# Performance work log

Hardware: AMD Instinct MI355X
Metric: run time of the kernel (lower is better)

## Reference

```python
import jax, jax.numpy as jnp
import numpy as np

B, S, H = 2, 2048, 2048
NUM_HEADS, HEAD_DIM, GROUP_SIZE = 16, 128, 4
NUM_KV_HEADS = NUM_HEADS // GROUP_SIZE
ROPE_THETA = 10000.0


def setup_inputs() -> dict:
    key = jax.random.key(0)
    ks = jax.random.split(key, 10)
    xavier = lambda k, fi, fo: jax.random.uniform(k, (fi, fo), jnp.float32,
                                                  -jnp.sqrt(6.0 / (fi + fo)), jnp.sqrt(6.0 / (fi + fo)))
    hidden_states = jax.random.normal(ks[0], (B, S, H), jnp.float32)
    # causal mask: 1.0 where attention is disallowed (strictly upper triangle)
    mask = jnp.triu(jnp.ones((S, S), jnp.float32), k=1)[None, None, :, :]
    mask = jnp.broadcast_to(mask, (B, 1, S, S))
    return {
        "hidden_states": hidden_states,
        "mask": mask,
        "Wq": xavier(ks[1], H, NUM_HEADS * HEAD_DIM), "bq": jnp.zeros((NUM_HEADS * HEAD_DIM,), jnp.float32),
        "Wk": xavier(ks[2], H, NUM_KV_HEADS * HEAD_DIM), "bk": jnp.zeros((NUM_KV_HEADS * HEAD_DIM,), jnp.float32),
        "Wv": xavier(ks[3], H, NUM_KV_HEADS * HEAD_DIM), "bv": jnp.zeros((NUM_KV_HEADS * HEAD_DIM,), jnp.float32),
        "Wo": xavier(ks[4], NUM_HEADS * HEAD_DIM, H), "bo": jnp.zeros((H,), jnp.float32),
    }


def _apply_rope(q, k):
    # q: [b, s, hq, d], k: [b, s, hk, d]
    s, d = q.shape[1], q.shape[-1]
    inv_freq = 1.0 / (ROPE_THETA ** (jnp.arange(0, d, 2, dtype=jnp.float32) / d))  # [d/2]
    angles = jnp.arange(s, dtype=jnp.float32)[:, None] * inv_freq[None, :]          # [s, d/2]
    cos = jnp.cos(angles)[None, :, None, :]  # [1, s, 1, d/2]
    sin = jnp.sin(angles)[None, :, None, :]

    def rot(x):
        x1, x2 = jnp.split(x, 2, axis=-1)
        return jnp.concatenate([x1 * cos - x2 * sin, x1 * sin + x2 * cos], axis=-1)

    return rot(q), rot(k)


def reference(hidden_states, mask, Wq, bq, Wk, bk, Wv, bv, Wo, bo):
    b, s, _ = hidden_states.shape
    scale = 1.0 / jnp.sqrt(jnp.float32(HEAD_DIM))

    q = (hidden_states @ Wq + bq).reshape(b, s, NUM_HEADS, HEAD_DIM)
    k = (hidden_states @ Wk + bk).reshape(b, s, NUM_KV_HEADS, HEAD_DIM)
    v = (hidden_states @ Wv + bv).reshape(b, s, NUM_KV_HEADS, HEAD_DIM)

    q, k = _apply_rope(q, k)

    q = jnp.transpose(q, (0, 2, 1, 3))  # [b, hq, s, d]
    k = jnp.transpose(k, (0, 2, 1, 3))  # [b, hk, s, d]
    v = jnp.transpose(v, (0, 2, 1, 3))

    new_past_key, new_past_value = k, v

    # GQA: repeat each KV head group_size times
    k_rep = jnp.repeat(k, GROUP_SIZE, axis=1)  # [b, hq, s, d]
    v_rep = jnp.repeat(v, GROUP_SIZE, axis=1)

    attn_scores = jnp.einsum('bhqd,bhkd->bhqk', q, k_rep) * scale  # [b, hq, s, s]
    attn_scores = attn_scores + mask * -1e9
    attn_probs = jax.nn.softmax(attn_scores, axis=-1)
    attn_output = jnp.einsum('bhqk,bhkd->bhqd', attn_probs, v_rep)

    attn_output = attn_output.transpose(0, 2, 1, 3).reshape(b, s, NUM_HEADS * HEAD_DIM)
    attn_output = attn_output @ Wo + bo
    return attn_output, new_past_key, new_past_value
```

## Files before the change

### kernel.cpp

```cpp
#include <hip/hip_runtime.h>
#include <stdint.h>

#define S_LEN 2048
#define HDIM  2048
#define N_HEADS 16
#define HEAD_D 128
#define N_KV 4

typedef unsigned short u16;
typedef __attribute__((ext_vector_type(8))) short bf16x8;
typedef __attribute__((ext_vector_type(4))) short bf16x4;
typedef __attribute__((ext_vector_type(4))) float f32x4;

#define MFMA_PV(a, b, c) __builtin_amdgcn_mfma_f32_16x16x16bf16_1k(a, b, c, 0, 0, 0)

__device__ __forceinline__ u16 f2bf(float f) {
  unsigned u = __float_as_uint(f);
  u += 0x7FFFu + ((u >> 16) & 1u);
  return (u16)(u >> 16);
}

__device__ __forceinline__ void gll16(void* lds, const void* gp) {
  __builtin_amdgcn_global_load_lds(
      (const __attribute__((address_space(1))) void*)gp,
      (__attribute__((address_space(3))) void*)lds, 16, 0, 0);
}

__global__ __launch_bounds__(256) void k_convert(const float* __restrict__ src,
                                                 u16* __restrict__ dst, int n4) {
  int i = blockIdx.x * 256 + threadIdx.x;
  if (i < n4) {
    float4 v = ((const float4*)src)[i];
    ushort4 o;
    o.x = f2bf(v.x); o.y = f2bf(v.y); o.z = f2bf(v.z); o.w = f2bf(v.w);
    ((ushort4*)dst)[i] = o;
  }
}

__global__ __launch_bounds__(256) void k_transpose_w(const float* __restrict__ W,
                                                     u16* __restrict__ Wt,
                                                     int K, int N) {
  __shared__ float tile[64][65];
  int k0 = blockIdx.x * 64, n0 = blockIdx.y * 64;
  int tr = threadIdx.x >> 6, tc = threadIdx.x & 63;
#pragma unroll
  for (int i = 0; i < 16; ++i) {
    int r = tr + i * 4;
    tile[r][tc] = W[(size_t)(k0 + r) * N + n0 + tc];
  }
  __syncthreads();
#pragma unroll
  for (int i = 0; i < 16; ++i) {
    int r = tr + i * 4;
    Wt[(size_t)(n0 + r) * K + k0 + tc] = f2bf(tile[tc][r]);
  }
}

__device__ __forceinline__ void gemm_tile_128(
    const u16* __restrict__ A, const u16* __restrict__ Bt,
    const float* __restrict__ bias, float* __restrict__ C,
    int m0, int n0, int K, int ldc) {
  __shared__ __align__(16) u16 sA[128 * 32];
  __shared__ __align__(16) u16 sB[128 * 32];
  const int tid = threadIdx.x;
  const int lane = tid & 63;
  const int wave = tid >> 6;
  const int quad = lane >> 4;
  const int l15 = lane & 15;
  const int wm = (wave >> 1) << 6;
  const int wn = (wave & 1) << 6;

  f32x4 acc[4][4];
#pragma unroll
  for (int i = 0; i < 4; ++i)
#pragma unroll
    for (int j = 0; j < 4; ++j)
      acc[i][j] = (f32x4){0.f, 0.f, 0.f, 0.f};

  for (int kk = 0; kk < K; kk += 32) {
    __syncthreads();
#pragma unroll
    for (int it = 0; it < 2; ++it) {
      int c = tid + (it << 8);
      int row = c >> 2;
      int ko = (c & 3) << 3;
      gll16((char*)sA + c * 16, A + (size_t)(m0 + row) * K + kk + ko);
      gll16((char*)sB + c * 16, Bt + (size_t)(n0 + row) * K + kk + ko);
    }
    __syncthreads();
    bf16x8 af[4], bfr[4];
#pragma unroll
    for (int i = 0; i < 4; ++i)
      af[i] = *(const bf16x8*)&sA[(wm + (i << 4) + l15) * 32 + quad * 8];
#pragma unroll
    for (int j = 0; j < 4; ++j)
      bfr[j] = *(const bf16x8*)&sB[(wn + (j << 4) + l15) * 32 + quad * 8];
#pragma unroll
    for (int i = 0; i < 4; ++i)
#pragma unroll
      for (int j = 0; j < 4; ++j)
        acc[i][j] = __builtin_amdgcn_mfma_f32_16x16x32_bf16(af[i], bfr[j], acc[i][j], 0, 0, 0);
  }

#pragma unroll
  for (int i = 0; i < 4; ++i) {
    int row = m0 + wm + (i << 4) + quad * 4;
#pragma unroll
    for (int j = 0; j < 4; ++j) {
      int col = n0 + wn + (j << 4) + l15;
      float bv = bias[col];
      float* cp = C + (size_t)row * ldc + col;
#pragma unroll
      for (int r = 0; r < 4; ++r)
        cp[(size_t)r * ldc] = acc[i][j][r] + bv;
    }
  }
}

__global__ __launch_bounds__(256) void k_gemm_qkv(
    const u16* __restrict__ X, const u16* __restrict__ Wqt,
    const u16* __restrict__ Wkt, const u16* __restrict__ Wvt,
    const float* __restrict__ bq, const float* __restrict__ bk,
    const float* __restrict__ bv, float* __restrict__ Qf,
    float* __restrict__ Kf, float* __restrict__ Vf) {
  int m0 = blockIdx.x << 7;
  int by = blockIdx.y;
  const u16* Bt; const float* bias; float* C; int n0, ldc;
  if (by < 16)      { Bt = Wqt; bias = bq; C = Qf; n0 = by << 7;        ldc = 2048; }
  else if (by < 20) { Bt = Wkt; bias = bk; C = Kf; n0 = (by - 16) << 7; ldc = 512;  }
  else              { Bt = Wvt; bias = bv; C = Vf; n0 = (by - 20) << 7; ldc = 512;  }
  gemm_tile_128(X, Bt, bias, C, m0, n0, 2048, ldc);
}

__global__ __launch_bounds__(256) void k_gemm_o(
    const u16* __restrict__ A, const u16* __restrict__ Wot,
    const float* __restrict__ bo, float* __restrict__ C) {
  gemm_tile_128(A, Wot, bo, C, blockIdx.x << 7, blockIdx.y << 7, 2048, 2048);
}

__global__ __launch_bounds__(256) void k_rope(
    const float* __restrict__ Qf, const float* __restrict__ Kf,
    u16* __restrict__ Qbf, u16* __restrict__ Kbf, float* __restrict__ outK) {
  const int bx = blockIdx.x;
  const int b = bx >> 11;
  const int s = bx & 2047;
  const int tid = threadIdx.x;
  const float qscale = 0.08838834764831845f * 1.4426950408889634f;
  const float c1 = -13.287712379549449f / 64.f;

#pragma unroll
  for (int it = 0; it < 4; ++it) {
    int p = tid + (it << 8);
    int hh = p >> 6;
    int ii = p & 63;
    float ang = (float)s * exp2f((float)ii * c1);
    float cs, sn;
    sincosf(ang, &sn, &cs);
    const float* src = Qf + (size_t)bx * 2048 + hh * 128 + ii;
    float x1 = src[0], x2 = src[64];
    float o1 = (x1 * cs - x2 * sn) * qscale;
    float o2 = (x1 * sn + x2 * cs) * qscale;
    u16* dst = Qbf + ((size_t)(b * N_HEADS + hh) * S_LEN + s) * HEAD_D + ii;
    dst[0] = f2bf(o1);
    dst[64] = f2bf(o2);
  }
  {
    int hh = tid >> 6;
    int ii = tid & 63;
    float ang = (float)s * exp2f((float)ii * c1);
    float cs, sn;
    sincosf(ang, &sn, &cs);
    const float* src = Kf + (size_t)bx * 512 + hh * 128 + ii;
    float x1 = src[0], x2 = src[64];
    float o1 = x1 * cs - x2 * sn;
    float o2 = x1 * sn + x2 * cs;
    size_t idx = ((size_t)(b * N_KV + hh) * S_LEN + s) * HEAD_D + ii;
    Kbf[idx] = f2bf(o1);
    Kbf[idx + 64] = f2bf(o2);
    outK[idx] = o1;
    outK[idx + 64] = o2;
  }
}

__global__ __launch_bounds__(256) void k_vtrans(const float* __restrict__ Vf,
                                                u16* __restrict__ Vt,
                                                float* __restrict__ outV) {
  __shared__ float tile[64][65];
  int s0 = blockIdx.x * 64, d0 = blockIdx.y * 64;
  int z = blockIdx.z;
  int b = z >> 2, kvh = z & 3;
  int tr = threadIdx.x >> 6, tc = threadIdx.x & 63;
#pragma unroll
  for (int i = 0; i < 16; ++i) {
    int r = tr + i * 4;
    float v = Vf[(size_t)(b * S_LEN + s0 + r) * 512 + kvh * 128 + d0 + tc];
    tile[r][tc] = v;
    outV[((size_t)z * S_LEN + s0 + r) * HEAD_D + d0 + tc] = v;
  }
  __syncthreads();
#pragma unroll
  for (int i = 0; i < 16; ++i) {
    int r = tr + i * 4;
    Vt[((size_t)z * HEAD_D + d0 + r) * S_LEN + s0 + tc] = f2bf(tile[tc][r]);
  }
}

__global__ __launch_bounds__(256, 2) void k_attn(
    const u16* __restrict__ Qbf, const u16* __restrict__ Kbf,
    const u16* __restrict__ Vt, u16* __restrict__ attn) {
  __shared__ __align__(16) u16 smem[17920];
  u16* sK = smem;
  u16* sV = smem + 8704;

  const int tid = threadIdx.x;
  const int lane = tid & 63;
  const int wave = tid >> 6;
  const int quad = lane >> 4;
  const int l15 = lane & 15;

  const int by = blockIdx.y;
  const int qt = (by < 8) ? (15 - 2 * by) : (2 * (by - 8));
  const int bh = blockIdx.x;
  const int b = bh >> 4;
  const int h = bh & 15;
  const int kvh = h >> 2;
  const int q0 = qt << 7;
  const int qw = q0 + wave * 32;

  const u16* Qb = Qbf + ((size_t)(b * N_HEADS + h) * S_LEN + qw) * HEAD_D;
  const u16* Kb = Kbf + (size_t)(b * N_KV + kvh) * S_LEN * HEAD_D;
  const u16* Vb = Vt + (size_t)(b * N_KV + kvh) * HEAD_D * S_LEN;

  bf16x8 aq[2][4];
#pragma unroll
  for (int i = 0; i < 2; ++i)
#pragma unroll
    for (int kc = 0; kc < 4; ++kc)
      aq[i][kc] = *(const bf16x8*)(Qb + (size_t)(i * 16 + l15) * HEAD_D + kc * 32 + quad * 8);

  float mst[2] = {-1e30f, -1e30f}, lst[2] = {0.f, 0.f};
  f32x4 oacc[2][8];
#pragma unroll
  for (int i = 0; i < 2; ++i)
#pragma unroll
    for (int n = 0; n < 8; ++n) oacc[i][n] = (f32x4){0.f, 0.f, 0.f, 0.f};

  const int ntiles = 2 * qt + 2;
  for (int t = 0; t < ntiles; ++t) {
    const int kt0 = t << 6;
    __syncthreads();
#pragma unroll
    for (int it = 0; it < 9; ++it) {
      int c = tid + (it << 8);
      if (c < 1088) {
        int row = c / 17;
        int k16 = c - row * 17;
        gll16((char*)sK + c * 16, Kb + (size_t)(kt0 + row) * HEAD_D + k16 * 8);
      } else if (c < 2240) {
        int vv = c - 1088;
        int d = vv / 9;
        int s16 = vv - d * 9;
        gll16((char*)sV + vv * 16, Vb + (size_t)d * S_LEN + kt0 + s16 * 8);
      }
    }
    __syncthreads();

    if (kt0 > qw + 31) continue;

    f32x4 st[2][4];
#pragma unroll
    for (int i = 0; i < 2; ++i)
#pragma unroll
      for (int j = 0; j < 4; ++j) st[i][j] = (f32x4){0.f, 0.f, 0.f, 0.f};
#pragma unroll
    for (int kc = 0; kc < 4; ++kc) {
#pragma unroll
      for (int j = 0; j < 4; ++j) {
        bf16x8 kf = *(const bf16x8*)&sK[(j * 16 + l15) * 136 + kc * 32 + quad * 8];
#pragma unroll
        for (int i = 0; i < 2; ++i)
          st[i][j] = __builtin_amdgcn_mfma_f32_16x16x32_bf16(kf, aq[i][kc], st[i][j], 0, 0, 0);
      }
    }

    if (kt0 + 63 > qw) {
#pragma unroll
      for (int i = 0; i < 2; ++i) {
        int q = qw + i * 16 + l15;
#pragma unroll
        for (int j = 0; j < 4; ++j) {
          int s = kt0 + j * 16 + quad * 4;
#pragma unroll
          for (int r = 0; r < 4; ++r)
            if (s + r > q) st[i][j][r] = -1e9f;
        }
      }
    }

    bf16x4 pf[2][4];
    float al[2];
#pragma unroll
    for (int i = 0; i < 2; ++i) {
      float m = -1e30f;
#pragma unroll
      for (int j = 0; j < 4; ++j)
#pragma unroll
        for (int r = 0; r < 4; ++r) m = fmaxf(m, st[i][j][r]);
      m = fmaxf(m, __shfl_xor(m, 16, 64));
      m = fmaxf(m, __shfl_xor(m, 32, 64));
      float mn = fmaxf(mst[i], m);
      al[i] = exp2f(mst[i] - mn);
      mst[i] = mn;
      float rs = 0.f;
#pragma unroll
      for (int j = 0; j < 4; ++j) {
#pragma unroll
        for (int r = 0; r < 4; ++r) {
          float p = exp2f(st[i][j][r] - mn);
          rs += p;
          pf[i][j][r] = (short)f2bf(p);
        }
      }
      rs += __shfl_xor(rs, 16, 64);
      rs += __shfl_xor(rs, 32, 64);
      lst[i] = lst[i] * al[i] + rs;
#pragma unroll
      for (int r = 0; r < 4; ++r) {
        float a = __shfl(al[i], quad * 4 + r, 16);
#pragma unroll
        for (int n = 0; n < 8; ++n) oacc[i][n][r] *= a;
      }
    }

#pragma unroll
    for (int j = 0; j < 4; ++j) {
#pragma unroll
      for (int n = 0; n < 8; ++n) {
        bf16x4 vf = *(const bf16x4*)&sV[(n * 16 + l15) * 72 + j * 16 + quad * 4];
#pragma unroll
        for (int i = 0; i < 2; ++i)
          oacc[i][n] = MFMA_PV(pf[i][j], vf, oacc[i][n]);
      }
    }
  }

#pragma unroll
  for (int i = 0; i < 2; ++i)
#pragma unroll
    for (int r = 0; r < 4; ++r) {
      float inv = 1.0f / __shfl(lst[i], quad * 4 + r, 16);
      int row = qw + i * 16 + quad * 4 + r;
      u16* op = attn + ((size_t)b * S_LEN + row) * HDIM + h * HEAD_D;
#pragma unroll
      for (int n = 0; n < 8; ++n)
        op[n * 16 + l15] = f2bf(oacc[i][n][r] * inv);
    }
}

extern "C" void kernel_launch(void* const* d_in, const int* in_sizes, int n_in,
                              void* d_out, int out_size, void* d_ws, size_t ws_size,
                              hipStream_t stream) {
  (void)in_sizes; (void)n_in; (void)out_size; (void)ws_size;
  const float* hs = (const float*)d_in[0];
  const float* Wq = (const float*)d_in[2];
  const float* bq = (const float*)d_in[3];
  const float* Wk = (const float*)d_in[4];
  const float* bk = (const float*)d_in[5];
  const float* Wv = (const float*)d_in[6];
  const float* bv = (const float*)d_in[7];
  const float* Wo = (const float*)d_in[8];
  const float* bo = (const float*)d_in[9];
  float* out = (float*)d_out;

  char* ws = (char*)d_ws;
  u16* Xbf   = (u16*)(ws + 0);
  u16* Wqt   = (u16*)(ws + 16777216);
  u16* Wkt   = (u16*)(ws + 25165824);
  u16* Wvt   = (u16*)(ws + 27262976);
  u16* Wot   = (u16*)(ws + 29360128);
  float* Qf  = (float*)(ws + 37748736);
  float* Kf  = (float*)(ws + 71303168);
  float* Vf  = (float*)(ws + 79691776);
  u16* Qbf   = (u16*)(ws + 88080384);
  u16* Kbf   = (u16*)(ws + 104857600);
  u16* Vtb   = (u16*)(ws + 109051904);
  u16* attnb = (u16*)(ws + 37748736);

  k_convert<<<8192, 256, 0, stream>>>(hs, Xbf, 2097152);
  k_transpose_w<<<dim3(32, 32), 256, 0, stream>>>(Wq, Wqt, 2048, 2048);
  k_transpose_w<<<dim3(32, 8), 256, 0, stream>>>(Wk, Wkt, 2048, 512);
  k_transpose_w<<<dim3(32, 8), 256, 0, stream>>>(Wv, Wvt, 2048, 512);
  k_transpose_w<<<dim3(32, 32), 256, 0, stream>>>(Wo, Wot, 2048, 2048);
  k_gemm_qkv<<<dim3(32, 24), 256, 0, stream>>>(Xbf, Wqt, Wkt, Wvt, bq, bk, bv, Qf, Kf, Vf);
  k_rope<<<4096, 256, 0, stream>>>(Qf, Kf, Qbf, Kbf, out + 8388608);
  k_vtrans<<<dim3(32, 2, 8), 256, 0, stream>>>(Vf, Vtb, out + 10485760);
  k_attn<<<dim3(32, 16), 256, 0, stream>>>(Qbf, Kbf, Vtb, attnb);
  k_gemm_o<<<dim3(32, 16), 256, 0, stream>>>(attnb, Wot, bo, out);
}
```

Measured before the change: 374.8 us.

## Split long causal attention tiles across two blocks and merge partials

Query tiles 8-15, which have the longest causal KV ranges, are split into two KV halves processed by separate blocks. Each half writes unnormalized bf16 partial outputs plus running max and sum, and a new combine kernel merges them. This balances the work per block and gives more blocks to fill the GPU. The cost is an extra kernel launch, partial-output traffic, and bf16 rounding of the partials. Separately, the softmax probabilities are now packed to bf16 with perm and round-half-up instead of round-to-nearest-even.

```diff
diff --git a/kernel.cpp b/kernel.cpp
--- a/kernel.cpp
+++ b/kernel.cpp
@@ -18,6 +18,10 @@
   unsigned u = __float_as_uint(f);
   u += 0x7FFFu + ((u >> 16) & 1u);
   return (u16)(u >> 16);
+}
+
+__device__ __forceinline__ float bf2f(u16 v) {
+  return __uint_as_float(((unsigned)v) << 16);
 }
 
 __device__ __forceinline__ void gll16(void* lds, const void* gp) {
@@ -207,7 +211,8 @@
 
 __global__ __launch_bounds__(256, 2) void k_attn(
     const u16* __restrict__ Qbf, const u16* __restrict__ Kbf,
-    const u16* __restrict__ Vt, u16* __restrict__ attn) {
+    const u16* __restrict__ Vt, u16* __restrict__ attn,
+    u16* __restrict__ pO, float* __restrict__ pML) {
   __shared__ __align__(16) u16 smem[17920];
   u16* sK = smem;
   u16* sV = smem + 8704;
@@ -219,7 +224,21 @@
   const int l15 = lane & 15;
 
   const int by = blockIdx.y;
-  const int qt = (by < 8) ? (15 - 2 * by) : (2 * (by - 8));
+  int qt, t0, t1, slot;
+  bool finalw;
+  if (by < 8) {
+    qt = 8 + by; t0 = 0; t1 = 16; finalw = false;
+    slot = ((blockIdx.x << 3) + (qt - 8)) << 1;
+  } else {
+    qt = 23 - by;
+    if (qt >= 8) {
+      t0 = 16; t1 = 2 * qt + 2; finalw = false;
+      slot = (((blockIdx.x << 3) + (qt - 8)) << 1) + 1;
+    } else {
+      t0 = 0; t1 = 2 * qt + 2; finalw = true; slot = 0;
+    }
+  }
+
   const int bh = blockIdx.x;
   const int b = bh >> 4;
   const int h = bh & 15;
@@ -245,8 +264,7 @@
 #pragma unroll
     for (int n = 0; n < 8; ++n) oacc[i][n] = (f32x4){0.f, 0.f, 0.f, 0.f};
 
-  const int ntiles = 2 * qt + 2;
-  for (int t = 0; t < ntiles; ++t) {
+  for (int t = t0; t < t1; ++t) {
     const int kt0 = t << 6;
     __syncthreads();
 #pragma unroll
@@ -314,12 +332,17 @@
       float rs = 0.f;
 #pragma unroll
       for (int j = 0; j < 4; ++j) {
-#pragma unroll
-        for (int r = 0; r < 4; ++r) {
-          float p = exp2f(st[i][j][r] - mn);
-          rs += p;
-          pf[i][j][r] = (short)f2bf(p);
-        }
+        float p0 = exp2f(st[i][j][0] - mn);
+        float p1 = exp2f(st[i][j][1] - mn);
+        float p2 = exp2f(st[i][j][2] - mn);
+        float p3 = exp2f(st[i][j][3] - mn);
+        rs += (p0 + p1) + (p2 + p3);
+        union { unsigned u[2]; bf16x4 v; } pk;
+        pk.u[0] = __builtin_amdgcn_perm(__float_as_uint(p1) + 0x8000u,
+                                        __float_as_uint(p0) + 0x8000u, 0x07060302u);
+        pk.u[1] = __builtin_amdgcn_perm(__float_as_uint(p3) + 0x8000u,
+                                        __float_as_uint(p2) + 0x8000u, 0x07060302u);
+        pf[i][j] = pk.v;
       }
       rs += __shfl_xor(rs, 16, 64);
       rs += __shfl_xor(rs, 32, 64);
@@ -344,17 +367,82 @@
     }
   }
 
-#pragma unroll
-  for (int i = 0; i < 2; ++i)
-#pragma unroll
-    for (int r = 0; r < 4; ++r) {
-      float inv = 1.0f / __shfl(lst[i], quad * 4 + r, 16);
-      int row = qw + i * 16 + quad * 4 + r;
-      u16* op = attn + ((size_t)b * S_LEN + row) * HDIM + h * HEAD_D;
-#pragma unroll
-      for (int n = 0; n < 8; ++n)
-        op[n * 16 + l15] = f2bf(oacc[i][n][r] * inv);
-    }
+  if (finalw) {
+#pragma unroll
+    for (int i = 0; i < 2; ++i)
+#pragma unroll
+      for (int r = 0; r < 4; ++r) {
+        float inv = 1.0f / __shfl(lst[i], quad * 4 + r, 16);
+        int row = qw + i * 16 + quad * 4 + r;
+        u16* op = attn + ((size_t)b * S_LEN + row) * HDIM + h * HEAD_D;
+#pragma unroll
+        for (int n = 0; n < 8; ++n)
+          op[n * 16 + l15] = f2bf(oacc[i][n][r] * inv);
+      }
+  } else {
+    u16* po = pO + (size_t)slot * 16384;
+#pragma unroll
+    for (int i = 0; i < 2; ++i)
+#pragma unroll
+      for (int r = 0; r < 4; ++r) {
+        int row = wave * 32 + i * 16 + quad * 4 + r;
+#pragma unroll
+        for (int n = 0; n < 8; ++n)
+          po[row * 128 + n * 16 + l15] = f2bf(oacc[i][n][r]);
+      }
+    if (quad == 0) {
+      float* ml = pML + slot * 256;
+#pragma unroll
+      for (int i = 0; i < 2; ++i) {
+        int row = wave * 32 + i * 16 + l15;
+        ml[row] = mst[i];
+        ml[128 + row] = lst[i];
+      }
+    }
+  }
+}
+
+__global__ __launch_bounds__(256) void k_attn_combine(
+    const u16* __restrict__ pO, const float* __restrict__ pML,
+    u16* __restrict__ attn) {
+  const int bh = blockIdx.x;
+  const int qt = 8 + blockIdx.y;
+  const int b = bh >> 4;
+  const int h = bh & 15;
+  const int s0 = ((bh << 3) + blockIdx.y) << 1;
+  const int row = threadIdx.x >> 1;
+  const int half = threadIdx.x & 1;
+
+  const float* ml0 = pML + s0 * 256;
+  const float* ml1 = pML + (s0 + 1) * 256;
+  float m0 = ml0[row], l0 = ml0[128 + row];
+  float m1 = ml1[row], l1 = ml1[128 + row];
+  float m = fmaxf(m0, m1);
+  float w0 = exp2f(m0 - m), w1 = exp2f(m1 - m);
+  float inv = 1.0f / (l0 * w0 + l1 * w1);
+  w0 *= inv; w1 *= inv;
+
+  const u16* o0 = pO + (size_t)s0 * 16384 + row * 128 + half * 64;
+  const u16* o1 = o0 + 16384;
+  u16* op = attn + ((size_t)(b * S_LEN + (qt << 7) + row)) * HDIM + h * HEAD_D + half * 64;
+#pragma unroll
+  for (int k = 0; k < 8; ++k) {
+    ushort4 a0 = ((const ushort4*)o0)[k * 2];
+    ushort4 b0 = ((const ushort4*)o0)[k * 2 + 1];
+    ushort4 a1 = ((const ushort4*)o1)[k * 2];
+    ushort4 b1 = ((const ushort4*)o1)[k * 2 + 1];
+    ushort4 ra, rb;
+    ra.x = f2bf(bf2f(a0.x) * w0 + bf2f(a1.x) * w1);
+    ra.y = f2bf(bf2f(a0.y) * w0 + bf2f(a1.y) * w1);
+    ra.z = f2bf(bf2f(a0.z) * w0 + bf2f(a1.z) * w1);
+    ra.w = f2bf(bf2f(a0.w) * w0 + bf2f(a1.w) * w1);
+    rb.x = f2bf(bf2f(b0.x) * w0 + bf2f(b1.x) * w1);
+    rb.y = f2bf(bf2f(b0.y) * w0 + bf2f(b1.y) * w1);
+    rb.z = f2bf(bf2f(b0.z) * w0 + bf2f(b1.z) * w1);
+    rb.w = f2bf(bf2f(b0.w) * w0 + bf2f(b1.w) * w1);
+    ((ushort4*)op)[k * 2] = ra;
+    ((ushort4*)op)[k * 2 + 1] = rb;
+  }
 }
 
 extern "C" void kernel_launch(void* const* d_in, const int* in_sizes, int n_in,
@@ -385,6 +473,8 @@
   u16* Kbf   = (u16*)(ws + 104857600);
   u16* Vtb   = (u16*)(ws + 109051904);
   u16* attnb = (u16*)(ws + 37748736);
+  float* pML = (float*)(ws + 54525952);
+  u16* pO    = (u16*)(ws + 71303168);
 
   k_convert<<<8192, 256, 0, stream>>>(hs, Xbf, 2097152);
   k_transpose_w<<<dim3(32, 32), 256, 0, stream>>>(Wq, Wqt, 2048, 2048);
@@ -394,6 +484,7 @@
   k_gemm_qkv<<<dim3(32, 24), 256, 0, stream>>>(Xbf, Wqt, Wkt, Wvt, bq, bk, bv, Qf, Kf, Vf);
   k_rope<<<4096, 256, 0, stream>>>(Qf, Kf, Qbf, Kbf, out + 8388608);
   k_vtrans<<<dim3(32, 2, 8), 256, 0, stream>>>(Vf, Vtb, out + 10485760);
-  k_attn<<<dim3(32, 16), 256, 0, stream>>>(Qbf, Kbf, Vtb, attnb);
+  k_attn<<<dim3(32, 24), 256, 0, stream>>>(Qbf, Kbf, Vtb, attnb, pO, pML);
+  k_attn_combine<<<dim3(32, 8), 256, 0, stream>>>(pO, pML, attnb);
   k_gemm_o<<<dim3(32, 16), 256, 0, stream>>>(attnb, Wot, bo, out);
 }
```

Result: no change. 367.8 us (-1.9%).
